# Kernel optimization log

Measured on AMD Instinct MI355X. Metric: run time of the kernel, lower is better.

The kernel has to match this reference:

```python
import jax, jax.numpy as jnp
import numpy as np

RADIUS = 8
EPS = 1e-4


def box_sum(mat, r):
    """Sliding (2r+1)x(2r+1) box sum with border truncation, via double cumsum.
    Operates on the last two axes; mat: [..., H, W]."""
    H, W = mat.shape[-2], mat.shape[-1]
    cs = jnp.cumsum(mat, axis=-2)
    d = jnp.concatenate([
        cs[..., r:2 * r + 1, :],                                   # rows [0, r]
        cs[..., 2 * r + 1:, :] - cs[..., :H - 2 * r - 1, :],       # rows [r+1, H-r)
        cs[..., -1:, :] - cs[..., H - 2 * r - 1:H - r - 1, :],     # rows [H-r, H)
    ], axis=-2)
    cs = jnp.cumsum(d, axis=-1)
    out = jnp.concatenate([
        cs[..., :, r:2 * r + 1],
        cs[..., :, 2 * r + 1:] - cs[..., :, :W - 2 * r - 1],
        cs[..., :, -1:] - cs[..., :, W - 2 * r - 1:W - r - 1],
    ], axis=-1)
    return out


def setup_inputs() -> dict:
    key = jax.random.key(0)
    k1, k2 = jax.random.split(key)
    shape = (1, 3, 4096, 4096)
    i = jax.random.uniform(k1, shape, dtype=jnp.float32)
    p = jax.random.uniform(k2, shape, dtype=jnp.float32)
    return {"i": i, "p": p}


def reference(i, p):
    r, eps = RADIUS, EPS
    H, W = i.shape[-2], i.shape[-1]
    # per-pixel window pixel count (border-truncated)
    N = box_sum(jnp.ones((H, W), dtype=i.dtype), r)  # [H, W], broadcasts over (1, C)
    mean_i = box_sum(i, r) / N
    mean_p = box_sum(p, r) / N
    mean_pi = box_sum(p * i, r) / N
    mean_ii = box_sum(i * i, r) / N
    cov_ip = mean_pi - mean_p * mean_i
    cov_ii = mean_ii - mean_i * mean_i
    a = cov_ip / (cov_ii + eps)
    b = mean_p - a * mean_i
    q = jnp.clip(a * i + b, 0.0, 1.0)
    return q
```

## Files before the change

kernel.cpp:

```cpp
#include <hip/hip_runtime.h>


#define HH   4096
#define WW   4096
#define CC   3
#define RAD  8
#define LOG2W 12
#define OUTW 48
#define ROWS 69
#define CS   86
#define RS   60
#define WPB  4
#define EPS  1e-4f

__device__ __forceinline__ void scan4(float si, float sp, float spi, float sii,
                                      float& a, float& b, float& c, float& d) {
    asm("v_mov_b32 %0, %4\n\t"
        "v_mov_b32 %1, %5\n\t"
        "v_mov_b32 %2, %6\n\t"
        "v_mov_b32 %3, %7\n\t"
        "v_add_f32_dpp %0, %0, %0 row_shr:1 row_mask:0xf bank_mask:0xf bound_ctrl:0\n\t"
        "v_add_f32_dpp %1, %1, %1 row_shr:1 row_mask:0xf bank_mask:0xf bound_ctrl:0\n\t"
        "v_add_f32_dpp %2, %2, %2 row_shr:1 row_mask:0xf bank_mask:0xf bound_ctrl:0\n\t"
        "v_add_f32_dpp %3, %3, %3 row_shr:1 row_mask:0xf bank_mask:0xf bound_ctrl:0\n\t"
        "v_add_f32_dpp %0, %0, %0 row_shr:2 row_mask:0xf bank_mask:0xf bound_ctrl:0\n\t"
        "v_add_f32_dpp %1, %1, %1 row_shr:2 row_mask:0xf bank_mask:0xf bound_ctrl:0\n\t"
        "v_add_f32_dpp %2, %2, %2 row_shr:2 row_mask:0xf bank_mask:0xf bound_ctrl:0\n\t"
        "v_add_f32_dpp %3, %3, %3 row_shr:2 row_mask:0xf bank_mask:0xf bound_ctrl:0\n\t"
        "v_add_f32_dpp %0, %0, %0 row_shr:4 row_mask:0xf bank_mask:0xf bound_ctrl:0\n\t"
        "v_add_f32_dpp %1, %1, %1 row_shr:4 row_mask:0xf bank_mask:0xf bound_ctrl:0\n\t"
        "v_add_f32_dpp %2, %2, %2 row_shr:4 row_mask:0xf bank_mask:0xf bound_ctrl:0\n\t"
        "v_add_f32_dpp %3, %3, %3 row_shr:4 row_mask:0xf bank_mask:0xf bound_ctrl:0\n\t"
        "v_add_f32_dpp %0, %0, %0 row_shr:8 row_mask:0xf bank_mask:0xf bound_ctrl:0\n\t"
        "v_add_f32_dpp %1, %1, %1 row_shr:8 row_mask:0xf bank_mask:0xf bound_ctrl:0\n\t"
        "v_add_f32_dpp %2, %2, %2 row_shr:8 row_mask:0xf bank_mask:0xf bound_ctrl:0\n\t"
        "v_add_f32_dpp %3, %3, %3 row_shr:8 row_mask:0xf bank_mask:0xf bound_ctrl:0\n\t"
        "v_add_f32_dpp %0, %0, %0 row_bcast:15 row_mask:0xa bank_mask:0xf\n\t"
        "v_add_f32_dpp %1, %1, %1 row_bcast:15 row_mask:0xa bank_mask:0xf\n\t"
        "v_add_f32_dpp %2, %2, %2 row_bcast:15 row_mask:0xa bank_mask:0xf\n\t"
        "v_add_f32_dpp %3, %3, %3 row_bcast:15 row_mask:0xa bank_mask:0xf\n\t"
        "v_add_f32_dpp %0, %0, %0 row_bcast:31 row_mask:0xc bank_mask:0xf\n\t"
        "v_add_f32_dpp %1, %1, %1 row_bcast:31 row_mask:0xc bank_mask:0xf\n\t"
        "v_add_f32_dpp %2, %2, %2 row_bcast:31 row_mask:0xc bank_mask:0xf\n\t"
        "v_add_f32_dpp %3, %3, %3 row_bcast:31 row_mask:0xc bank_mask:0xf"
        : "=&v"(a), "=&v"(b), "=&v"(c), "=&v"(d)
        : "v"(si), "v"(sp), "v"(spi), "v"(sii));
}

__device__ __forceinline__ float win17(float pref, int a_dn, int a_up, float nmsk) {
    float dn = __int_as_float(__builtin_amdgcn_ds_bpermute(a_dn, __float_as_int(pref)));
    float up = __int_as_float(__builtin_amdgcn_ds_bpermute(a_up, __float_as_int(pref)));
    return fmaf(nmsk, up, dn);
}

__global__ __launch_bounds__(256, 8)
void gf_stream_kernel(const float* __restrict__ gi,
                      const float* __restrict__ gp,
                      float* __restrict__ gq) {
    const int lane = threadIdx.x & 63;
    const int wid  = __builtin_amdgcn_readfirstlane(blockIdx.x * WPB + (threadIdx.x >> 6));

    const int c   = wid / (CS * RS);
    const int rm  = wid - c * (CS * RS);
    const int rs  = rm / CS;
    const int cs  = rm - rs * CS;
    const int x0  = cs * OUTW;
    const int y0  = rs * ROWS;

    const size_t plane = (size_t)HH << LOG2W;
    const float* Ic = gi + (size_t)c * plane;
    const float* Pc = gp + (size_t)c * plane;
    float*       Qc = gq + (size_t)c * plane;

    const int  gx    = x0 - RAD + lane;
    const bool colok = (gx >= 0) && (gx < WW);
    const int  gxc   = min(max(gx, 0), WW - 1);
    const bool outl  = (lane >= RAD) && (lane < RAD + OUTW) && (gx < WW);
    const int  a_dn  = ((lane + RAD) & 63) << 2;
    const int  a_up  = ((lane - RAD - 1) & 63) << 2;
    const float nmsk = (lane >= RAD + 1) ? -1.0f : 0.0f;

    const int   nx     = min(gx + RAD, WW - 1) - max(gx - RAD, 0) + 1;
    const float inv_nx = __builtin_amdgcn_rcpf((float)max(nx, 1));

    float bi[17], bp[17];
    float si = 0.f, sp = 0.f, spi = 0.f, sii = 0.f;

#pragma unroll
    for (int k = 0; k < 17; ++k) {
        int y = y0 - RAD + k;
        float a = 0.f, b = 0.f;
        if (y >= 0 && y < HH) {
            const float* rI = Ic + ((size_t)(unsigned)y << LOG2W);
            const float* rP = Pc + ((size_t)(unsigned)y << LOG2W);
            float av = rI[gxc];
            float bv = rP[gxc];
            a = colok ? av : 0.f;
            b = colok ? bv : 0.f;
        }
        bi[k] = a; bp[k] = b;
        si += a; sp += b; spi += a * b; sii += a * a;
    }

    auto emit = [&](int y, float icur) {
        float Si, Sp, Spi, Sii;
        scan4(si, sp, spi, sii, Si, Sp, Spi, Sii);
        float wi  = win17(Si,  a_dn, a_up, nmsk);
        float wp  = win17(Sp,  a_dn, a_up, nmsk);
        float wpi = win17(Spi, a_dn, a_up, nmsk);
        float wii = win17(Sii, a_dn, a_up, nmsk);

        int   ny   = min(y + RAD, HH - 1) - max(y - RAD, 0) + 1;
        float invN = inv_nx * __builtin_amdgcn_rcpf((float)ny);
        float mi   = wi  * invN;
        float mp   = wp  * invN;
        float mpi  = wpi * invN;
        float mii  = wii * invN;
        float cip  = fmaf(-mp, mi, mpi);
        float cii  = fmaf(-mi, mi, mii);
        float a    = cip * __builtin_amdgcn_rcpf(cii + EPS);
        float b    = fmaf(-a, mi, mp);
        float q    = __builtin_amdgcn_fmed3f(fmaf(a, icur, b), 0.0f, 1.0f);
        if (outl) {
            float* Qrow = Qc + ((size_t)(unsigned)y << LOG2W);
            Qrow[gx] = q;
        }
    };

    emit(y0, bi[8]);

    int y = y0;
#pragma unroll 1
    for (int o = 0; o < 4; ++o) {
#pragma unroll
        for (int u = 0; u < 17; ++u) {
            ++y;
            float a0 = bi[u], b0 = bp[u];
            si -= a0; sp -= b0;
            spi = fmaf(-a0, b0, spi);
            sii = fmaf(-a0, a0, sii);

            int yin = y + RAD;
            float a = 0.f, b = 0.f;
            if (yin < HH) {
                const float* rI = Ic + ((size_t)(unsigned)yin << LOG2W);
                const float* rP = Pc + ((size_t)(unsigned)yin << LOG2W);
                float av = rI[gxc];
                float bv = rP[gxc];
                a = colok ? av : 0.f;
                b = colok ? bv : 0.f;
            }
            bi[u] = a; bp[u] = b;
            si += a; sp += b;
            spi = fmaf(a, b, spi);
            sii = fmaf(a, a, sii);

            if (y < HH)
                emit(y, bi[(u + 9) % 17]);
        }
    }
}

extern "C" void kernel_launch(void* const* d_in, const int* in_sizes, int n_in,
                              void* d_out, int out_size, void* d_ws, size_t ws_size,
                              hipStream_t stream) {
    const float* gi = (const float*)d_in[0];
    const float* gp = (const float*)d_in[1];
    float* gq = (float*)d_out;
    const int total_waves = CC * CS * RS;
    const int blocks = total_waves / WPB;
    gf_stream_kernel<<<blocks, 256, 0, stream>>>(gi, gp, gq);
}
```

Measured before the change: 497.8 us.

## Process two columns per lane with float2 loads and prefetch next row

```diff
diff --git a/kernel.cpp b/kernel.cpp
--- a/kernel.cpp
+++ b/kernel.cpp
@@ -1,15 +1,18 @@
 #include <hip/hip_runtime.h>
 
+
+typedef float v2f __attribute__((ext_vector_type(2)));
 
 #define HH   4096
 #define WW   4096
 #define CC   3
 #define RAD  8
 #define LOG2W 12
-#define OUTW 48
-#define ROWS 69
-#define CS   86
-#define RS   60
+#define OUTC 112
+#define ROWS 35
+#define CS   37
+#define RS   118
+#define TOTALW (CC*CS*RS)
 #define WPB  4
 #define EPS  1e-4f
 
@@ -47,24 +50,23 @@
         : "v"(si), "v"(sp), "v"(spi), "v"(sii));
 }
 
-__device__ __forceinline__ float win17(float pref, int a_dn, int a_up, float nmsk) {
-    float dn = __int_as_float(__builtin_amdgcn_ds_bpermute(a_dn, __float_as_int(pref)));
-    float up = __int_as_float(__builtin_amdgcn_ds_bpermute(a_up, __float_as_int(pref)));
-    return fmaf(nmsk, up, dn);
-}
-
-__global__ __launch_bounds__(256, 8)
+__device__ __forceinline__ float bper(int addr, float x) {
+    return __int_as_float(__builtin_amdgcn_ds_bpermute(addr, __float_as_int(x)));
+}
+
+__global__ __launch_bounds__(256, 4)
 void gf_stream_kernel(const float* __restrict__ gi,
                       const float* __restrict__ gp,
                       float* __restrict__ gq) {
     const int lane = threadIdx.x & 63;
     const int wid  = __builtin_amdgcn_readfirstlane(blockIdx.x * WPB + (threadIdx.x >> 6));
+    if (wid >= TOTALW) return;
 
     const int c   = wid / (CS * RS);
     const int rm  = wid - c * (CS * RS);
     const int rs  = rm / CS;
     const int cs  = rm - rs * CS;
-    const int x0  = cs * OUTW;
+    const int xb  = cs * OUTC - RAD;
     const int y0  = rs * ROWS;
 
     const size_t plane = (size_t)HH << LOG2W;
@@ -72,58 +74,104 @@
     const float* Pc = gp + (size_t)c * plane;
     float*       Qc = gq + (size_t)c * plane;
 
-    const int  gx    = x0 - RAD + lane;
-    const bool colok = (gx >= 0) && (gx < WW);
-    const int  gxc   = min(max(gx, 0), WW - 1);
-    const bool outl  = (lane >= RAD) && (lane < RAD + OUTW) && (gx < WW);
-    const int  a_dn  = ((lane + RAD) & 63) << 2;
-    const int  a_up  = ((lane - RAD - 1) & 63) << 2;
-    const float nmsk = (lane >= RAD + 1) ? -1.0f : 0.0f;
-
-    const int   nx     = min(gx + RAD, WW - 1) - max(gx - RAD, 0) + 1;
-    const float inv_nx = __builtin_amdgcn_rcpf((float)max(nx, 1));
-
-    float bi[17], bp[17];
-    float si = 0.f, sp = 0.f, spi = 0.f, sii = 0.f;
+    const int  gx0 = xb + 2 * lane;
+    const bool pv  = (gx0 >= 0) && (gx0 < WW);
+    const int  gxc = min(max(gx0, 0), WW - 2);
+    const bool outok = (lane >= 4) && (lane < 60) && pv;
+
+    const int   adn = ((lane + 4) & 63) << 2;
+    const int   au5 = ((lane - 5) & 63) << 2;
+    const int   au4 = ((lane - 4) & 63) << 2;
+    const float m5  = (lane >= 5) ? -1.0f : 0.0f;
+    const float m4  = (lane >= 4) ? -1.0f : 0.0f;
+
+    const int gx1 = gx0 + 1;
+    const int nx0 = min(gx0 + RAD, WW - 1) - max(gx0 - RAD, 0) + 1;
+    const int nx1 = min(gx1 + RAD, WW - 1) - max(gx1 - RAD, 0) + 1;
+    v2f invnx;
+    invnx.x = __builtin_amdgcn_rcpf((float)max(nx0, 1));
+    invnx.y = __builtin_amdgcn_rcpf((float)max(nx1, 1));
+
+    const v2f zero = {0.f, 0.f};
+    v2f bi[17], bp[17];
+    v2f vsi = zero, vsp = zero, vspi = zero, vsii = zero;
 
 #pragma unroll
     for (int k = 0; k < 17; ++k) {
-        int y = y0 - RAD + k;
-        float a = 0.f, b = 0.f;
-        if (y >= 0 && y < HH) {
-            const float* rI = Ic + ((size_t)(unsigned)y << LOG2W);
-            const float* rP = Pc + ((size_t)(unsigned)y << LOG2W);
-            float av = rI[gxc];
-            float bv = rP[gxc];
-            a = colok ? av : 0.f;
-            b = colok ? bv : 0.f;
+        int yy = y0 - RAD + k;
+        v2f a = zero, b = zero;
+        if (yy >= 0 && yy < HH) {
+            const float* rI = Ic + ((size_t)(unsigned)yy << LOG2W);
+            const float* rP = Pc + ((size_t)(unsigned)yy << LOG2W);
+            v2f av = *reinterpret_cast<const v2f*>(rI + gxc);
+            v2f bv = *reinterpret_cast<const v2f*>(rP + gxc);
+            a = pv ? av : zero;
+            b = pv ? bv : zero;
         }
         bi[k] = a; bp[k] = b;
-        si += a; sp += b; spi += a * b; sii += a * a;
+        vsi += a; vsp += b;
+        vspi = __builtin_elementwise_fma(a, b, vspi);
+        vsii = __builtin_elementwise_fma(a, a, vsii);
     }
 
-    auto emit = [&](int y, float icur) {
-        float Si, Sp, Spi, Sii;
-        scan4(si, sp, spi, sii, Si, Sp, Spi, Sii);
-        float wi  = win17(Si,  a_dn, a_up, nmsk);
-        float wp  = win17(Sp,  a_dn, a_up, nmsk);
-        float wpi = win17(Spi, a_dn, a_up, nmsk);
-        float wii = win17(Sii, a_dn, a_up, nmsk);
-
-        int   ny   = min(y + RAD, HH - 1) - max(y - RAD, 0) + 1;
-        float invN = inv_nx * __builtin_amdgcn_rcpf((float)ny);
-        float mi   = wi  * invN;
-        float mp   = wp  * invN;
-        float mpi  = wpi * invN;
-        float mii  = wii * invN;
-        float cip  = fmaf(-mp, mi, mpi);
-        float cii  = fmaf(-mi, mi, mii);
-        float a    = cip * __builtin_amdgcn_rcpf(cii + EPS);
-        float b    = fmaf(-a, mi, mp);
-        float q    = __builtin_amdgcn_fmed3f(fmaf(a, icur, b), 0.0f, 1.0f);
-        if (outl) {
+    v2f pfa = zero, pfb = zero;
+    {
+        int py = y0 + RAD + 1;
+        if (py < HH) {
+            const float* rI = Ic + ((size_t)(unsigned)py << LOG2W);
+            const float* rP = Pc + ((size_t)(unsigned)py << LOG2W);
+            pfa = *reinterpret_cast<const v2f*>(rI + gxc);
+            pfb = *reinterpret_cast<const v2f*>(rP + gxc);
+        }
+    }
+
+    auto emit = [&](int y, v2f icur) {
+        float psi  = vsi.x  + vsi.y;
+        float psp  = vsp.x  + vsp.y;
+        float pspi = vspi.x + vspi.y;
+        float psii = vsii.x + vsii.y;
+        float Pi_, Pp_, Ppi_, Pii_;
+        scan4(psi, psp, pspi, psii, Pi_, Pp_, Ppi_, Pii_);
+        float Qi_  = Pi_  - vsi.y;
+        float Qp_  = Pp_  - vsp.y;
+        float Qpi_ = Ppi_ - vspi.y;
+        float Qii_ = Pii_ - vsii.y;
+
+        auto taps = [&](float P_, float Q_) -> v2f {
+            float qdn = bper(adn, Q_);
+            float pdn = bper(adn, P_);
+            float pu5 = bper(au5, P_);
+            float qu4 = bper(au4, Q_);
+            v2f w;
+            w.x = fmaf(m5, pu5, qdn);
+            w.y = fmaf(m4, qu4, pdn);
+            return w;
+        };
+        v2f wi  = taps(Pi_,  Qi_);
+        v2f wp  = taps(Pp_,  Qp_);
+        v2f wpi = taps(Ppi_, Qpi_);
+        v2f wii = taps(Pii_, Qii_);
+
+        int   ny  = min(y + RAD, HH - 1) - max(y - RAD, 0) + 1;
+        float iny = __builtin_amdgcn_rcpf((float)ny);
+        v2f invN  = invnx * iny;
+        v2f mi  = wi  * invN;
+        v2f mp  = wp  * invN;
+        v2f mpi = wpi * invN;
+        v2f mii = wii * invN;
+        v2f cip = __builtin_elementwise_fma(-mp, mi, mpi);
+        v2f cii = __builtin_elementwise_fma(-mi, mi, mii);
+        v2f den = cii + EPS;
+        v2f ra;
+        ra.x = __builtin_amdgcn_rcpf(den.x);
+        ra.y = __builtin_amdgcn_rcpf(den.y);
+        v2f aa = cip * ra;
+        v2f bb = __builtin_elementwise_fma(-aa, mi, mp);
+        v2f q  = __builtin_elementwise_fma(aa, icur, bb);
+        q = __builtin_elementwise_min(__builtin_elementwise_max(q, zero), (v2f){1.f, 1.f});
+        if (outok) {
             float* Qrow = Qc + ((size_t)(unsigned)y << LOG2W);
-            Qrow[gx] = q;
+            *reinterpret_cast<v2f*>(Qrow + gx0) = q;
         }
     };
 
@@ -131,29 +179,29 @@
 
     int y = y0;
 #pragma unroll 1
-    for (int o = 0; o < 4; ++o) {
+    for (int o = 0; o < 2; ++o) {
 #pragma unroll
         for (int u = 0; u < 17; ++u) {
             ++y;
-            float a0 = bi[u], b0 = bp[u];
-            si -= a0; sp -= b0;
-            spi = fmaf(-a0, b0, spi);
-            sii = fmaf(-a0, a0, sii);
-
-            int yin = y + RAD;
-            float a = 0.f, b = 0.f;
-            if (yin < HH) {
-                const float* rI = Ic + ((size_t)(unsigned)yin << LOG2W);
-                const float* rP = Pc + ((size_t)(unsigned)yin << LOG2W);
-                float av = rI[gxc];
-                float bv = rP[gxc];
-                a = colok ? av : 0.f;
-                b = colok ? bv : 0.f;
-            }
-            bi[u] = a; bp[u] = b;
-            si += a; sp += b;
-            spi = fmaf(a, b, spi);
-            sii = fmaf(a, a, sii);
+            v2f a0 = bi[u], b0 = bp[u];
+            vsi -= a0; vsp -= b0;
+            vspi = __builtin_elementwise_fma(-a0, b0, vspi);
+            vsii = __builtin_elementwise_fma(-a0, a0, vsii);
+
+            v2f na = pv ? pfa : zero;
+            v2f nb = pv ? pfb : zero;
+            bi[u] = na; bp[u] = nb;
+            vsi += na; vsp += nb;
+            vspi = __builtin_elementwise_fma(na, nb, vspi);
+            vsii = __builtin_elementwise_fma(na, na, vsii);
+
+            int py = y + RAD + 1;
+            if (py < HH) {
+                const float* rI = Ic + ((size_t)(unsigned)py << LOG2W);
+                const float* rP = Pc + ((size_t)(unsigned)py << LOG2W);
+                pfa = *reinterpret_cast<const v2f*>(rI + gxc);
+                pfb = *reinterpret_cast<const v2f*>(rP + gxc);
+            } else { pfa = zero; pfb = zero; }
 
             if (y < HH)
                 emit(y, bi[(u + 9) % 17]);
@@ -167,7 +215,6 @@
     const float* gi = (const float*)d_in[0];
     const float* gp = (const float*)d_in[1];
     float* gq = (float*)d_out;
-    const int total_waves = CC * CS * RS;
-    const int blocks = total_waves / WPB;
+    const int blocks = (TOTALW + WPB - 1) / WPB;
     gf_stream_kernel<<<blocks, 256, 0, stream>>>(gi, gp, gq);
 }
```

After: 512.9 us. +3.0%, slower.
